# Optimization experiments

Measured on AMD Instinct MI355X. Metric: run time of the kernel, lower is better.

Reference implementation:

```python
import jax, jax.numpy as jnp
import numpy as np

N_NODES = 50000
N_EDGES = 800000
N_FEAT = 128
N_HID = 64


def setup_inputs() -> dict:
    key = jax.random.key(0)
    k1, k2, k3, k4, k5, k6, k7 = jax.random.split(key, 7)
    x = jax.random.normal(k1, (N_NODES, N_FEAT), dtype=jnp.float32)
    edge_index = jax.random.randint(k2, (2, N_EDGES), 0, N_NODES, dtype=jnp.int64)
    edge_weight = jax.random.uniform(k3, (N_EDGES,), dtype=jnp.float32)
    # GraphConvolution params (Glorot-ish scaling)
    w1 = jax.random.normal(k4, (N_FEAT, N_HID), dtype=jnp.float32) / np.sqrt(N_FEAT)
    b1 = jnp.zeros((N_HID,), dtype=jnp.float32)
    w2 = jax.random.normal(k5, (N_HID, N_HID), dtype=jnp.float32) / np.sqrt(N_HID)
    b2 = jnp.zeros((N_HID,), dtype=jnp.float32)
    return {"x": x, "edge_index": edge_index, "edge_weight": edge_weight,
            "w1": w1, "b1": b1, "w2": w2, "b2": b2}


def _gcn_layer(h, src, dst, edge_weight, w, b, n_nodes):
    # GraphConvolution: adj @ (h @ w) + b, adj given as weighted edge list
    hw = h @ w                                   # [N, H]
    msgs = hw[src] * edge_weight[:, None]        # [E, H] gather + scale
    agg = jax.ops.segment_sum(msgs, dst, num_segments=n_nodes)  # [N, H]
    return agg + b


def reference(x, edge_index, edge_weight, w1, b1, w2, b2):
    src, dst = edge_index[0], edge_index[1]
    h = jax.nn.relu(_gcn_layer(x, src, dst, edge_weight, w1, b1, N_NODES))
    # dropout is identity in eval mode
    out = _gcn_layer(h, src, dst, edge_weight, w2, b2, N_NODES)
    return out
```

## Files before the change

kernel.cpp:

```cpp
#include <hip/hip_runtime.h>

#define N_NODES 50000
#define N_EDGES 800000
#define N_FEAT  128
#define N_HID   64

#define BKT_LOG 9
#define BKT_SZ  512
#define NBKT    ((N_NODES + BKT_SZ - 1) / BKT_SZ)
#define CH      4096
#define NB1     ((N_EDGES + CH - 1) / CH)
#define GROWS   64
#define GG      ((N_NODES + GROWS - 1) / GROWS)
#define AGG_B   2048

__device__ inline void fma4(float4& acc, float s, const float4& w) {
    acc.x = fmaf(s, w.x, acc.x);
    acc.y = fmaf(s, w.y, acc.y);
    acc.z = fmaf(s, w.z, acc.z);
    acc.w = fmaf(s, w.w, acc.w);
}

__device__ inline unsigned short f2bf(float f) {
    unsigned u = __float_as_uint(f);
    u = u + 0x7FFFu + ((u >> 16) & 1u);
    return (unsigned short)(u >> 16);
}

__device__ inline int wave_incl_scan(int v) {
    int lane = threadIdx.x & 63;
#pragma unroll
    for (int o = 1; o < 64; o <<= 1) {
        int u = __shfl_up(v, o);
        if (lane >= o) v += u;
    }
    return v;
}

__device__ inline void fma_bf8(float4& lo, float4& hi, float w, const uint4& v) {
    lo.x = fmaf(w, __uint_as_float(v.x << 16), lo.x);
    lo.y = fmaf(w, __uint_as_float(v.x & 0xFFFF0000u), lo.y);
    lo.z = fmaf(w, __uint_as_float(v.y << 16), lo.z);
    lo.w = fmaf(w, __uint_as_float(v.y & 0xFFFF0000u), lo.w);
    hi.x = fmaf(w, __uint_as_float(v.z << 16), hi.x);
    hi.y = fmaf(w, __uint_as_float(v.z & 0xFFFF0000u), hi.y);
    hi.z = fmaf(w, __uint_as_float(v.w << 16), hi.z);
    hi.w = fmaf(w, __uint_as_float(v.w & 0xFFFF0000u), hi.w);
}

template <int K>
__device__ inline void gemm_body(const float* __restrict__ a, const float* __restrict__ lw,
                                 unsigned short* __restrict__ o, int blk) {
    int tid = threadIdx.x;
    int rp = tid >> 3;
    int c0 = (tid & 7) * 8;
    int row0 = blk * GROWS + rp * 2;
    if (row0 >= N_NODES) return;
    bool two = (row0 + 1) < N_NODES;

    const float* a0 = a + (long)row0 * K;
    const float* a1 = two ? (a0 + K) : a0;

    float4 aA0 = make_float4(0.f, 0.f, 0.f, 0.f), aA1 = aA0;
    float4 aB0 = aA0, aB1 = aA0;

#pragma unroll 4
    for (int k4 = 0; k4 < K / 4; ++k4) {
        float4 xa = *(const float4*)(a0 + k4 * 4);
        float4 xb = *(const float4*)(a1 + k4 * 4);
#pragma unroll
        for (int j = 0; j < 4; ++j) {
            const float* wk = &lw[(k4 * 4 + j) * N_HID + c0];
            float4 w0 = *(const float4*)(wk);
            float4 w1 = *(const float4*)(wk + 4);
            float sa = (j == 0) ? xa.x : (j == 1) ? xa.y : (j == 2) ? xa.z : xa.w;
            float sb = (j == 0) ? xb.x : (j == 1) ? xb.y : (j == 2) ? xb.z : xb.w;
            fma4(aA0, sa, w0); fma4(aA1, sa, w1);
            fma4(aB0, sb, w0); fma4(aB1, sb, w1);
        }
    }

    unsigned short* op = o + (long)row0 * N_HID + c0;
    *(ushort4*)op = make_ushort4(f2bf(aA0.x), f2bf(aA0.y), f2bf(aA0.z), f2bf(aA0.w));
    *(ushort4*)(op + 4) = make_ushort4(f2bf(aA1.x), f2bf(aA1.y), f2bf(aA1.z), f2bf(aA1.w));
    if (two) {
        *(ushort4*)(op + N_HID) = make_ushort4(f2bf(aB0.x), f2bf(aB0.y), f2bf(aB0.z), f2bf(aB0.w));
        *(ushort4*)(op + N_HID + 4) = make_ushort4(f2bf(aB1.x), f2bf(aB1.y), f2bf(aB1.z), f2bf(aB1.w));
    }
}

__global__ __launch_bounds__(256) void gemm1_hist(const float* __restrict__ a,
                                                  const float* __restrict__ w,
                                                  unsigned short* __restrict__ o,
                                                  const int* __restrict__ dst,
                                                  int* __restrict__ cnt,
                                                  int* __restrict__ cnt_t) {
    __shared__ float lw[N_FEAT * N_HID];
    int tid = threadIdx.x;
    if (blockIdx.x < NB1) {
        int* h = (int*)lw;
        int bid = blockIdx.x;
        if (tid < NBKT) h[tid] = 0;
        __syncthreads();
        int e0 = bid * CH;
        for (int i = tid; i < CH; i += 256) {
            int e = e0 + i;
            if (e < N_EDGES) atomicAdd(&h[dst[e] >> BKT_LOG], 1);
        }
        __syncthreads();
        if (tid < NBKT) {
            int v = h[tid];
            cnt[bid * NBKT + tid] = v;
            cnt_t[tid * NB1 + bid] = v;
        }
        return;
    }
    for (int idx = tid * 4; idx < N_FEAT * N_HID; idx += 256 * 4)
        *(float4*)&lw[idx] = *(const float4*)&w[idx];
    __syncthreads();
    gemm_body<N_FEAT>(a, lw, o, blockIdx.x - NB1);
}

__global__ __launch_bounds__(256) void gemm2_bf16(const unsigned short* __restrict__ a,
                                                  const float* __restrict__ w,
                                                  unsigned short* __restrict__ o) {
    __shared__ float lw[N_HID * N_HID];
    int tid = threadIdx.x;
    for (int idx = tid * 4; idx < N_HID * N_HID; idx += 256 * 4)
        *(float4*)&lw[idx] = *(const float4*)&w[idx];
    __syncthreads();

    int rp = tid >> 3;
    int c0 = (tid & 7) * 8;
    int row0 = blockIdx.x * GROWS + rp * 2;
    if (row0 >= N_NODES) return;
    bool two = (row0 + 1) < N_NODES;

    const unsigned short* a0 = a + (long)row0 * N_HID;
    const unsigned short* a1 = two ? (a0 + N_HID) : a0;

    float4 aA0 = make_float4(0.f, 0.f, 0.f, 0.f), aA1 = aA0;
    float4 aB0 = aA0, aB1 = aA0;

#pragma unroll 2
    for (int k8 = 0; k8 < N_HID / 8; ++k8) {
        uint4 xa = *(const uint4*)(a0 + k8 * 8);
        uint4 xb = *(const uint4*)(a1 + k8 * 8);
        float sa[8], sb[8];
        sa[0] = __uint_as_float(xa.x << 16); sa[1] = __uint_as_float(xa.x & 0xFFFF0000u);
        sa[2] = __uint_as_float(xa.y << 16); sa[3] = __uint_as_float(xa.y & 0xFFFF0000u);
        sa[4] = __uint_as_float(xa.z << 16); sa[5] = __uint_as_float(xa.z & 0xFFFF0000u);
        sa[6] = __uint_as_float(xa.w << 16); sa[7] = __uint_as_float(xa.w & 0xFFFF0000u);
        sb[0] = __uint_as_float(xb.x << 16); sb[1] = __uint_as_float(xb.x & 0xFFFF0000u);
        sb[2] = __uint_as_float(xb.y << 16); sb[3] = __uint_as_float(xb.y & 0xFFFF0000u);
        sb[4] = __uint_as_float(xb.z << 16); sb[5] = __uint_as_float(xb.z & 0xFFFF0000u);
        sb[6] = __uint_as_float(xb.w << 16); sb[7] = __uint_as_float(xb.w & 0xFFFF0000u);
#pragma unroll
        for (int j = 0; j < 8; ++j) {
            const float* wk = &lw[(k8 * 8 + j) * N_HID + c0];
            float4 w0 = *(const float4*)(wk);
            float4 w1 = *(const float4*)(wk + 4);
            fma4(aA0, sa[j], w0); fma4(aA1, sa[j], w1);
            fma4(aB0, sb[j], w0); fma4(aB1, sb[j], w1);
        }
    }

    unsigned short* op = o + (long)row0 * N_HID + c0;
    *(ushort4*)op = make_ushort4(f2bf(aA0.x), f2bf(aA0.y), f2bf(aA0.z), f2bf(aA0.w));
    *(ushort4*)(op + 4) = make_ushort4(f2bf(aA1.x), f2bf(aA1.y), f2bf(aA1.z), f2bf(aA1.w));
    if (two) {
        *(ushort4*)(op + N_HID) = make_ushort4(f2bf(aB0.x), f2bf(aB0.y), f2bf(aB0.z), f2bf(aB0.w));
        *(ushort4*)(op + N_HID + 4) = make_ushort4(f2bf(aB1.x), f2bf(aB1.y), f2bf(aB1.z), f2bf(aB1.w));
    }
}

__global__ __launch_bounds__(256) void binscatter(const int* __restrict__ src,
                                                  const int* __restrict__ dst,
                                                  const float* __restrict__ ew,
                                                  const int* __restrict__ cnt,
                                                  const int* __restrict__ cnt_t,
                                                  uint2* __restrict__ slab) {
    __shared__ int cur[NBKT];
    __shared__ int wtot[2];
    int t = threadIdx.x;
    int b = blockIdx.x;

    int tot = 0, pre = 0;
    if (t < NBKT) {
        const int4* p = (const int4*)(cnt_t + t * NB1);
        for (int q = 0; q < NB1 / 4; ++q) {
            int4 v = p[q];
            tot += v.x + v.y + v.z + v.w;
        }
        int p0 = 0, p1 = 0, p2 = 0, p3 = 0;
        int j = 0;
        for (; j + 4 <= b; j += 4) {
            p0 += cnt[(j + 0) * NBKT + t];
            p1 += cnt[(j + 1) * NBKT + t];
            p2 += cnt[(j + 2) * NBKT + t];
            p3 += cnt[(j + 3) * NBKT + t];
        }
        for (; j < b; ++j) p0 += cnt[j * NBKT + t];
        pre = p0 + p1 + p2 + p3;
    }
    int incl = wave_incl_scan(tot);
    if (t < 128 && (t & 63) == 63) wtot[t >> 6] = incl;
    __syncthreads();
    if (t < NBKT) {
        int bstart_t = (t >= 64 ? wtot[0] : 0) + incl - tot;
        cur[t] = bstart_t + pre;
    }
    __syncthreads();

    int e0 = b * CH;
    for (int i = t; i < CH; i += 256) {
        int e = e0 + i;
        if (e >= N_EDGES) continue;
        int d = dst[e];
        int bin = d >> BKT_LOG;
        int p = atomicAdd(&cur[bin], 1);
        slab[p] = make_uint2((unsigned)src[e] | ((unsigned)(d & (BKT_SZ - 1)) << 16),
                             __float_as_uint(ew[e]));
    }
}

__global__ __launch_bounds__(512) void sort_bucket(const uint2* __restrict__ slab,
                                                   const int* __restrict__ cnt_t,
                                                   unsigned* __restrict__ edges,
                                                   int* __restrict__ start) {
    __shared__ int tt[NBKT];
    __shared__ int h[BKT_SZ];
    __shared__ int wtot[8];
    __shared__ int bs[2];
    int b = blockIdx.x;
    int t = threadIdx.x;
    int lane = t & 63;
    int w = t >> 6;

    if (t < NBKT) {
        int s = 0;
        const int4* p = (const int4*)(cnt_t + t * NB1);
        for (int q = 0; q < NB1 / 4; ++q) {
            int4 v = p[q];
            s += v.x + v.y + v.z + v.w;
        }
        tt[t] = s;
    }
    __syncthreads();
    if (t < 64) {
        int v = (t < b ? tt[t] : 0) + (t + 64 < b ? tt[t + 64] : 0);
#pragma unroll
        for (int o = 32; o >= 1; o >>= 1) v += __shfl_xor(v, o);
        if (t == 0) { bs[0] = v; bs[1] = tt[b]; }
    }
    __syncthreads();
    int base = bs[0];
    int c = bs[1];

    h[t] = 0;
    __syncthreads();
    for (int i = t; i < c; i += 512)
        atomicAdd(&h[(slab[base + i].x >> 16) & (BKT_SZ - 1)], 1);
    __syncthreads();

    int v = h[t];
    int incl = wave_incl_scan(v);
    if (lane == 63) wtot[w] = incl;
    __syncthreads();
    int add = 0;
#pragma unroll
    for (int i = 0; i < 8; ++i) add += (i < w) ? wtot[i] : 0;
    int excl = add + incl - v;

    int g = (b << BKT_LOG) + t;
    if (g < N_NODES) start[g] = base + excl;
    if (b == NBKT - 1 && t == 0) start[N_NODES] = N_EDGES;

    h[t] = base + excl;
    __syncthreads();
    for (int i = t; i < c; i += 512) {
        uint2 r = slab[base + i];
        int p = atomicAdd(&h[(r.x >> 16) & (BKT_SZ - 1)], 1);
        edges[p] = (r.x & 0xFFFFu) | ((unsigned)f2bf(__uint_as_float(r.y)) << 16);
    }
}

__device__ inline void agg_core8(const unsigned short* __restrict__ hwb,
                                 const unsigned* __restrict__ edges,
                                 int i0, int i1, int es, int f8,
                                 float4& lo, float4& hi) {
    lo = make_float4(0.f, 0.f, 0.f, 0.f);
    hi = lo;
    for (int base = i0; base < i1; base += 16) {
        int ia = base + es;
        int ib = base + 8 + es;
        float wa = 0.f, wb = 0.f;
        uint4 va = make_uint4(0u, 0u, 0u, 0u), vb = va;
        if (ia < i1) {
            unsigned e = edges[ia];
            wa = __uint_as_float(e & 0xFFFF0000u);
            va = *(const uint4*)&hwb[(long)(e & 0xFFFFu) * N_HID + f8];
        }
        if (ib < i1) {
            unsigned e = edges[ib];
            wb = __uint_as_float(e & 0xFFFF0000u);
            vb = *(const uint4*)&hwb[(long)(e & 0xFFFFu) * N_HID + f8];
        }
        fma_bf8(lo, hi, wa, va);
        fma_bf8(lo, hi, wb, vb);
    }
#pragma unroll
    for (int m = 8; m <= 32; m <<= 1) {
        lo.x += __shfl_xor(lo.x, m); lo.y += __shfl_xor(lo.y, m);
        lo.z += __shfl_xor(lo.z, m); lo.w += __shfl_xor(lo.w, m);
        hi.x += __shfl_xor(hi.x, m); hi.y += __shfl_xor(hi.y, m);
        hi.z += __shfl_xor(hi.z, m); hi.w += __shfl_xor(hi.w, m);
    }
}

__global__ __launch_bounds__(256) void agg_relu(const unsigned short* __restrict__ hwb,
                                                const unsigned* __restrict__ edges,
                                                const int* __restrict__ start,
                                                const float* __restrict__ b1,
                                                unsigned short* __restrict__ hb) {
    int tid = threadIdx.x;
    int lane = tid & 63;
    int es = lane >> 3;
    int f8 = (lane & 7) * 8;
    float4 bl = *(const float4*)&b1[f8];
    float4 bh = *(const float4*)&b1[f8 + 4];
    for (int n = blockIdx.x * 4 + (tid >> 6); n < N_NODES; n += AGG_B * 4) {
        float4 lo, hi;
        agg_core8(hwb, edges, start[n], start[n + 1], es, f8, lo, hi);
        if (es == 0) {
            lo.x = fmaxf(lo.x + bl.x, 0.f); lo.y = fmaxf(lo.y + bl.y, 0.f);
            lo.z = fmaxf(lo.z + bl.z, 0.f); lo.w = fmaxf(lo.w + bl.w, 0.f);
            hi.x = fmaxf(hi.x + bh.x, 0.f); hi.y = fmaxf(hi.y + bh.y, 0.f);
            hi.z = fmaxf(hi.z + bh.z, 0.f); hi.w = fmaxf(hi.w + bh.w, 0.f);
            uint4 p;
            p.x = (unsigned)f2bf(lo.x) | ((unsigned)f2bf(lo.y) << 16);
            p.y = (unsigned)f2bf(lo.z) | ((unsigned)f2bf(lo.w) << 16);
            p.z = (unsigned)f2bf(hi.x) | ((unsigned)f2bf(hi.y) << 16);
            p.w = (unsigned)f2bf(hi.z) | ((unsigned)f2bf(hi.w) << 16);
            *(uint4*)&hb[(long)n * N_HID + f8] = p;
        }
    }
}

__global__ __launch_bounds__(256) void agg_out(const unsigned short* __restrict__ hwb2,
                                               const unsigned* __restrict__ edges,
                                               const int* __restrict__ start,
                                               const float* __restrict__ b2,
                                               float* __restrict__ o) {
    int tid = threadIdx.x;
    int lane = tid & 63;
    int es = lane >> 3;
    int f8 = (lane & 7) * 8;
    float4 bl = *(const float4*)&b2[f8];
    float4 bh = *(const float4*)&b2[f8 + 4];
    for (int n = blockIdx.x * 4 + (tid >> 6); n < N_NODES; n += AGG_B * 4) {
        float4 lo, hi;
        agg_core8(hwb2, edges, start[n], start[n + 1], es, f8, lo, hi);
        if (es == 0) {
            lo.x += bl.x; lo.y += bl.y; lo.z += bl.z; lo.w += bl.w;
            hi.x += bh.x; hi.y += bh.y; hi.z += bh.z; hi.w += bh.w;
            *(float4*)&o[(long)n * N_HID + f8] = lo;
            *(float4*)&o[(long)n * N_HID + f8 + 4] = hi;
        }
    }
}

extern "C" void kernel_launch(void* const* d_in, const int* in_sizes, int n_in,
                              void* d_out, int out_size, void* d_ws, size_t ws_size,
                              hipStream_t stream) {
    const float* x  = (const float*)d_in[0];
    const int*   ei = (const int*)d_in[1];
    const float* ew = (const float*)d_in[2];
    const float* w1 = (const float*)d_in[3];
    const float* b1 = (const float*)d_in[4];
    const float* w2 = (const float*)d_in[5];
    const float* b2 = (const float*)d_in[6];
    float* out = (float*)d_out;

    const int* src = ei;
    const int* dst = ei + N_EDGES;

    char* ws = (char*)d_ws;
    unsigned short* hwb  = (unsigned short*)ws;
    unsigned short* hwb2 = (unsigned short*)(ws + (size_t)7  * 1024 * 1024);
    unsigned short* hb   = (unsigned short*)(ws + (size_t)14 * 1024 * 1024);
    uint2*    slab  = (uint2*)   (ws + (size_t)21 * 1024 * 1024);
    unsigned* edges = (unsigned*)(ws + (size_t)28 * 1024 * 1024);
    int*      start = (int*)     (ws + (size_t)32 * 1024 * 1024);
    int*      cnt   = start + N_NODES + 8;
    int*      cnt_t = cnt + NB1 * NBKT;

    dim3 blk(256);

    gemm1_hist<<<dim3(NB1 + GG), blk, 0, stream>>>(x, w1, hwb, dst, cnt, cnt_t);
    binscatter<<<dim3(NB1), blk, 0, stream>>>(src, dst, ew, cnt, cnt_t, slab);
    sort_bucket<<<dim3(NBKT), dim3(512), 0, stream>>>(slab, cnt_t, edges, start);
    agg_relu<<<dim3(AGG_B), blk, 0, stream>>>(hwb, edges, start, b1, hb);
    gemm2_bf16<<<dim3(GG), blk, 0, stream>>>(hb, w2, hwb2);
    agg_out<<<dim3(AGG_B), blk, 0, stream>>>(hwb2, edges, start, b2, out);
}
```

Measured before the change: 112.2 us.

## Split feature tables into column halves with XCD-affine aggregation passes

Stores the bf16 hidden tables as two 32-column halves (split layout) instead of row-major 64 columns. The aggregation kernels now map blocks onto XCDs so that four XCDs gather from one half and four from the other. The goal is to shrink each XCD's gather working set so it fits in its local L2/cache and sees fewer misses. In exchange each edge index is read twice, and the mapping relies on round-robin placement of blocks onto XCDs.

Result: slower. 187.3 us (+66.9%).

```diff
diff --git a/kernel.cpp b/kernel.cpp
--- a/kernel.cpp
+++ b/kernel.cpp
@@ -4,6 +4,7 @@
 #define N_EDGES 800000
 #define N_FEAT  128
 #define N_HID   64
+#define HALF_STRIDE ((size_t)N_NODES * 32)
 
 #define BKT_LOG 9
 #define BKT_SZ  512
@@ -80,12 +81,12 @@
         }
     }
 
-    unsigned short* op = o + (long)row0 * N_HID + c0;
+    unsigned short* op = o + (size_t)(c0 >> 5) * HALF_STRIDE + (long)row0 * 32 + (c0 & 31);
     *(ushort4*)op = make_ushort4(f2bf(aA0.x), f2bf(aA0.y), f2bf(aA0.z), f2bf(aA0.w));
     *(ushort4*)(op + 4) = make_ushort4(f2bf(aA1.x), f2bf(aA1.y), f2bf(aA1.z), f2bf(aA1.w));
     if (two) {
-        *(ushort4*)(op + N_HID) = make_ushort4(f2bf(aB0.x), f2bf(aB0.y), f2bf(aB0.z), f2bf(aB0.w));
-        *(ushort4*)(op + N_HID + 4) = make_ushort4(f2bf(aB1.x), f2bf(aB1.y), f2bf(aB1.z), f2bf(aB1.w));
+        *(ushort4*)(op + 32) = make_ushort4(f2bf(aB0.x), f2bf(aB0.y), f2bf(aB0.z), f2bf(aB0.w));
+        *(ushort4*)(op + 36) = make_ushort4(f2bf(aB1.x), f2bf(aB1.y), f2bf(aB1.z), f2bf(aB1.w));
     }
 }
 
@@ -136,16 +137,15 @@
     if (row0 >= N_NODES) return;
     bool two = (row0 + 1) < N_NODES;
 
-    const unsigned short* a0 = a + (long)row0 * N_HID;
-    const unsigned short* a1 = two ? (a0 + N_HID) : a0;
-
     float4 aA0 = make_float4(0.f, 0.f, 0.f, 0.f), aA1 = aA0;
     float4 aB0 = aA0, aB1 = aA0;
 
-#pragma unroll 2
+#pragma unroll
     for (int k8 = 0; k8 < N_HID / 8; ++k8) {
-        uint4 xa = *(const uint4*)(a0 + k8 * 8);
-        uint4 xb = *(const uint4*)(a1 + k8 * 8);
+        const unsigned short* base = a + (size_t)(k8 >> 2) * HALF_STRIDE + (k8 & 3) * 8;
+        uint4 xa = *(const uint4*)(base + (long)row0 * 32);
+        uint4 xb = two ? *(const uint4*)(base + (long)(row0 + 1) * 32)
+                       : *(const uint4*)(base + (long)row0 * 32);
         float sa[8], sb[8];
         sa[0] = __uint_as_float(xa.x << 16); sa[1] = __uint_as_float(xa.x & 0xFFFF0000u);
         sa[2] = __uint_as_float(xa.y << 16); sa[3] = __uint_as_float(xa.y & 0xFFFF0000u);
@@ -165,12 +165,12 @@
         }
     }
 
-    unsigned short* op = o + (long)row0 * N_HID + c0;
+    unsigned short* op = o + (size_t)(c0 >> 5) * HALF_STRIDE + (long)row0 * 32 + (c0 & 31);
     *(ushort4*)op = make_ushort4(f2bf(aA0.x), f2bf(aA0.y), f2bf(aA0.z), f2bf(aA0.w));
     *(ushort4*)(op + 4) = make_ushort4(f2bf(aA1.x), f2bf(aA1.y), f2bf(aA1.z), f2bf(aA1.w));
     if (two) {
-        *(ushort4*)(op + N_HID) = make_ushort4(f2bf(aB0.x), f2bf(aB0.y), f2bf(aB0.z), f2bf(aB0.w));
-        *(ushort4*)(op + N_HID + 4) = make_ushort4(f2bf(aB1.x), f2bf(aB1.y), f2bf(aB1.z), f2bf(aB1.w));
+        *(ushort4*)(op + 32) = make_ushort4(f2bf(aB0.x), f2bf(aB0.y), f2bf(aB0.z), f2bf(aB0.w));
+        *(ushort4*)(op + 36) = make_ushort4(f2bf(aB1.x), f2bf(aB1.y), f2bf(aB1.z), f2bf(aB1.w));
     }
 }
 
@@ -285,32 +285,25 @@
     }
 }
 
-__device__ inline void agg_core8(const unsigned short* __restrict__ hwb,
-                                 const unsigned* __restrict__ edges,
-                                 int i0, int i1, int es, int f8,
-                                 float4& lo, float4& hi) {
+__device__ inline void agg_half(const unsigned short* __restrict__ tab,
+                                const unsigned* __restrict__ edges,
+                                int i0, int i1, int es, int f8,
+                                float4& lo, float4& hi) {
     lo = make_float4(0.f, 0.f, 0.f, 0.f);
     hi = lo;
     for (int base = i0; base < i1; base += 16) {
         int ia = base + es;
-        int ib = base + 8 + es;
-        float wa = 0.f, wb = 0.f;
-        uint4 va = make_uint4(0u, 0u, 0u, 0u), vb = va;
+        float wa = 0.f;
+        uint4 va = make_uint4(0u, 0u, 0u, 0u);
         if (ia < i1) {
             unsigned e = edges[ia];
             wa = __uint_as_float(e & 0xFFFF0000u);
-            va = *(const uint4*)&hwb[(long)(e & 0xFFFFu) * N_HID + f8];
-        }
-        if (ib < i1) {
-            unsigned e = edges[ib];
-            wb = __uint_as_float(e & 0xFFFF0000u);
-            vb = *(const uint4*)&hwb[(long)(e & 0xFFFFu) * N_HID + f8];
+            va = *(const uint4*)&tab[(long)(e & 0xFFFFu) * 32 + f8];
         }
         fma_bf8(lo, hi, wa, va);
-        fma_bf8(lo, hi, wb, vb);
-    }
-#pragma unroll
-    for (int m = 8; m <= 32; m <<= 1) {
+    }
+#pragma unroll
+    for (int m = 4; m <= 32; m <<= 1) {
         lo.x += __shfl_xor(lo.x, m); lo.y += __shfl_xor(lo.y, m);
         lo.z += __shfl_xor(lo.z, m); lo.w += __shfl_xor(lo.w, m);
         hi.x += __shfl_xor(hi.x, m); hi.y += __shfl_xor(hi.y, m);
@@ -325,13 +318,20 @@
                                                 unsigned short* __restrict__ hb) {
     int tid = threadIdx.x;
     int lane = tid & 63;
-    int es = lane >> 3;
-    int f8 = (lane & 7) * 8;
-    float4 bl = *(const float4*)&b1[f8];
-    float4 bh = *(const float4*)&b1[f8 + 4];
-    for (int n = blockIdx.x * 4 + (tid >> 6); n < N_NODES; n += AGG_B * 4) {
+    int wv = tid >> 6;
+    int es = lane >> 2;
+    int f8 = (lane & 3) * 8;
+    int xcd = blockIdx.x & 7;
+    int pass = xcd >> 2;
+    int sub = (blockIdx.x >> 3) * 4 + (xcd & 3);
+    const unsigned short* tab = hwb + (size_t)pass * HALF_STRIDE;
+    unsigned short* outp = hb + (size_t)pass * HALF_STRIDE;
+    float4 bl = *(const float4*)&b1[pass * 32 + f8];
+    float4 bh = *(const float4*)&b1[pass * 32 + f8 + 4];
+
+    for (int n = sub * 4 + wv; n < N_NODES; n += 4096) {
         float4 lo, hi;
-        agg_core8(hwb, edges, start[n], start[n + 1], es, f8, lo, hi);
+        agg_half(tab, edges, start[n], start[n + 1], es, f8, lo, hi);
         if (es == 0) {
             lo.x = fmaxf(lo.x + bl.x, 0.f); lo.y = fmaxf(lo.y + bl.y, 0.f);
             lo.z = fmaxf(lo.z + bl.z, 0.f); lo.w = fmaxf(lo.w + bl.w, 0.f);
@@ -342,7 +342,7 @@
             p.y = (unsigned)f2bf(lo.z) | ((unsigned)f2bf(lo.w) << 16);
             p.z = (unsigned)f2bf(hi.x) | ((unsigned)f2bf(hi.y) << 16);
             p.w = (unsigned)f2bf(hi.z) | ((unsigned)f2bf(hi.w) << 16);
-            *(uint4*)&hb[(long)n * N_HID + f8] = p;
+            *(uint4*)&outp[(long)n * 32 + f8] = p;
         }
     }
 }
@@ -354,18 +354,24 @@
                                                float* __restrict__ o) {
     int tid = threadIdx.x;
     int lane = tid & 63;
-    int es = lane >> 3;
-    int f8 = (lane & 7) * 8;
-    float4 bl = *(const float4*)&b2[f8];
-    float4 bh = *(const float4*)&b2[f8 + 4];
-    for (int n = blockIdx.x * 4 + (tid >> 6); n < N_NODES; n += AGG_B * 4) {
+    int wv = tid >> 6;
+    int es = lane >> 2;
+    int f8 = (lane & 3) * 8;
+    int xcd = blockIdx.x & 7;
+    int pass = xcd >> 2;
+    int sub = (blockIdx.x >> 3) * 4 + (xcd & 3);
+    const unsigned short* tab = hwb2 + (size_t)pass * HALF_STRIDE;
+    float4 bl = *(const float4*)&b2[pass * 32 + f8];
+    float4 bh = *(const float4*)&b2[pass * 32 + f8 + 4];
+
+    for (int n = sub * 4 + wv; n < N_NODES; n += 4096) {
         float4 lo, hi;
-        agg_core8(hwb2, edges, start[n], start[n + 1], es, f8, lo, hi);
+        agg_half(tab, edges, start[n], start[n + 1], es, f8, lo, hi);
         if (es == 0) {
             lo.x += bl.x; lo.y += bl.y; lo.z += bl.z; lo.w += bl.w;
             hi.x += bh.x; hi.y += bh.y; hi.z += bh.z; hi.w += bh.w;
-            *(float4*)&o[(long)n * N_HID + f8] = lo;
-            *(float4*)&o[(long)n * N_HID + f8 + 4] = hi;
+            *(float4*)&o[(long)n * N_HID + pass * 32 + f8] = lo;
+            *(float4*)&o[(long)n * N_HID + pass * 32 + f8 + 4] = hi;
         }
     }
 }
```
